# Optimization experiments

Measured on AMD Instinct MI355X. Metric: run time of the kernel, lower is better.

Reference implementation:

```python
import jax, jax.numpy as jnp
import numpy as np
from jax import lax

H = 1024      # hidden_size
E = 512       # embedding_size
K = 4         # max_num_children
NCLASS = 10000
EOS = NCLASS
N = 256       # number of tree nodes (complete K-ary tree, topo order)
L = 512       # number of annotation vectors


def setup_inputs() -> dict:
    key = jax.random.key(0)
    ks = jax.random.split(key, 16)
    s = 0.05
    rootH = jax.random.normal(ks[0], (1, H), jnp.float32)
    rootC = jax.random.normal(ks[1], (1, H), jnp.float32)
    annotations = jax.random.normal(ks[2], (L, H), jnp.float32)
    values = jax.random.randint(ks[3], (N,), 0, NCLASS, jnp.int32)
    idx = np.arange(N)
    parent = jnp.asarray(np.maximum(idx - 1, 0) // K, jnp.int32)
    slot = jnp.asarray(np.maximum(idx - 1, 0) % K, jnp.int32)
    # learned parameters
    emb = jax.random.normal(ks[4], (NCLASS + 1, E), jnp.float32) * s
    W_ih = jax.random.normal(ks[5], (K, 4 * H, E + H), jnp.float32) * s
    W_hh = jax.random.normal(ks[6], (K, 4 * H, H), jnp.float32) * s
    b_ih = jax.random.normal(ks[7], (K, 4 * H), jnp.float32) * s
    b_hh = jax.random.normal(ks[8], (K, 4 * H), jnp.float32) * s
    W_att = jax.random.normal(ks[9], (H, H), jnp.float32) * s
    b_att = jax.random.normal(ks[10], (H,), jnp.float32) * s
    W_pre = jax.random.normal(ks[11], (H, 2 * H), jnp.float32) * s
    b_pre = jax.random.normal(ks[12], (H,), jnp.float32) * s
    W_out = jax.random.normal(ks[13], (NCLASS + 1, H), jnp.float32) * s
    b_out = jax.random.normal(ks[14], (NCLASS + 1,), jnp.float32) * s
    return dict(rootH=rootH, rootC=rootC, annotations=annotations, values=values,
                parent=parent, slot=slot, emb=emb, W_ih=W_ih, W_hh=W_hh,
                b_ih=b_ih, b_hh=b_hh, W_att=W_att, b_att=b_att,
                W_pre=W_pre, b_pre=b_pre, W_out=W_out, b_out=b_out)


def reference(rootH, rootC, annotations, values, parent, slot, emb,
              W_ih, W_hh, b_ih, b_hh, W_att, b_att, W_pre, b_pre, W_out, b_out):
    # attention_hidden(annotations), computed once (align_type=1)
    ahv = annotations @ W_att.T + b_att            # [L, H]
    rootH0, rootC0 = rootH[0], rootC[0]            # [H]

    def step(carry, xs):
        Hbuf, Cbuf, etbuf, loss = carry
        i, v, p, k = xs
        # child LSTMCell update from parent state (slot k picks the cell)
        x = jnp.concatenate([emb[values[p]], etbuf[p]])            # [E+H]
        gates = W_ih[k] @ x + b_ih[k] + W_hh[k] @ Hbuf[p] + b_hh[k]  # [4H]
        ig, fg, gg, og = jnp.split(gates, 4)
        c_child = jax.nn.sigmoid(fg) * Cbuf[p] + jax.nn.sigmoid(ig) * jnp.tanh(gg)
        h_child = jax.nn.sigmoid(og) * jnp.tanh(c_child)
        is_root = i == 0
        h = jnp.where(is_root, rootH0, h_child)
        c = jnp.where(is_root, rootC0, c_child)
        # attention over annotations (softmax over L)
        att_logits = ahv @ h                                        # [L]
        probs = jax.nn.softmax(att_logits)
        ctx = probs @ annotations                                   # [H]
        et = jnp.tanh(W_pre @ jnp.concatenate([h, ctx]) + b_pre)    # [H]
        # output: softmax then CrossEntropyLoss (faithful double softmax)
        out_logits = W_out @ et + b_out                             # [NCLASS+1]
        p_out = jax.nn.softmax(out_logits)
        ls = jax.nn.log_softmax(p_out)
        nl = -ls[v]
        nl = jnp.where(v == EOS, nl / 5.0, nl)
        Hbuf = Hbuf.at[i].set(h)
        Cbuf = Cbuf.at[i].set(c)
        etbuf = etbuf.at[i].set(et)
        return (Hbuf, Cbuf, etbuf, loss + nl), None

    z = jnp.zeros((N, H), jnp.float32)
    init = (z, z, z, jnp.float32(0.0))
    xs = (jnp.arange(N, dtype=jnp.int32), values, parent, slot)
    (Hb, Cb, eb, loss), _ = lax.scan(step, init, xs)
    return loss
```

## Files before the change

### kernel.cpp

```cpp
#include <hip/hip_runtime.h>
#include <hip/hip_bf16.h>
#include <math.h>

#define HD 1024
#define NCLS 10001

typedef short s16x8 __attribute__((ext_vector_type(8)));
typedef unsigned short u16x8 __attribute__((ext_vector_type(8)));
typedef unsigned short u16x4 __attribute__((ext_vector_type(4)));
typedef float f32x4 __attribute__((ext_vector_type(4)));
#define MFMA16(a_, b_, c_) __builtin_amdgcn_mfma_f32_16x16x32_bf16((a_), (b_), (c_), 0, 0, 0)

__device__ __forceinline__ float sigf(float x){ return 1.f/(1.f+__expf(-x)); }
__device__ __forceinline__ float tanhfast(float x){
  x = fminf(fmaxf(x,-10.f),10.f);
  float e2 = __expf(2.f*x);
  return (e2-1.f)/(e2+1.f);
}
__device__ __forceinline__ unsigned short f2bf(float f){
  unsigned int u = __float_as_uint(f);
  u += 0x7FFF + ((u >> 16) & 1);
  return (unsigned short)(u >> 16);
}
__device__ __forceinline__ float bf2f(unsigned short u){
  return __uint_as_float(((unsigned)u) << 16);
}
__device__ __forceinline__ u16x8 pack8(float4 a, float4 b){
  u16x8 r;
  r[0]=f2bf(a.x); r[1]=f2bf(a.y); r[2]=f2bf(a.z); r[3]=f2bf(a.w);
  r[4]=f2bf(b.x); r[5]=f2bf(b.y); r[6]=f2bf(b.z); r[7]=f2bf(b.w);
  return r;
}

__global__ __launch_bounds__(256) void k_cvt32(const float* __restrict__ A, unsigned short* __restrict__ B, int n){
  int i = (blockIdx.x*256 + threadIdx.x)*32;
  if (i >= n) return;
  float4 a0 = *(const float4*)(A+i+ 0), b0 = *(const float4*)(A+i+ 4);
  float4 a1 = *(const float4*)(A+i+ 8), b1 = *(const float4*)(A+i+12);
  float4 a2 = *(const float4*)(A+i+16), b2 = *(const float4*)(A+i+20);
  float4 a3 = *(const float4*)(A+i+24), b3 = *(const float4*)(A+i+28);
  *(u16x8*)(B+i+ 0) = pack8(a0,b0);
  *(u16x8*)(B+i+ 8) = pack8(a1,b1);
  *(u16x8*)(B+i+16) = pack8(a2,b2);
  *(u16x8*)(B+i+24) = pack8(a3,b3);
}

__global__ __launch_bounds__(256) void k_cvtpre8(const float* __restrict__ Wpre,
                                                 unsigned short* __restrict__ Bpre, unsigned short* __restrict__ Wc){
  unsigned idx8 = (blockIdx.x*256 + threadIdx.x)*8;
  unsigned row = idx8 >> 11, c = idx8 & 2047;
  float4 a = *(const float4*)(Wpre + idx8);
  float4 b = *(const float4*)(Wpre + idx8 + 4);
  unsigned short* d = (c < 1024) ? (Bpre + (size_t)row*1536 + c) : (Wc + (size_t)row*1024 + (c-1024));
  *(u16x8*)d = pack8(a,b);
}

__global__ __launch_bounds__(256) void k_root(const float* __restrict__ rH, const float* __restrict__ rC,
                                              float* __restrict__ Hb, float* __restrict__ Cb,
                                              unsigned short* __restrict__ XH){
  int t = blockIdx.x*256 + threadIdx.x;
  if (t < HD){ Hb[t]=rH[t]; Cb[t]=rC[t]; XH[t]=f2bf(rH[t]); }
}

__global__ __launch_bounds__(256) void k_xasm(const float* __restrict__ emb, const int* __restrict__ values,
                                              const unsigned short* __restrict__ Etb, const unsigned short* __restrict__ XH,
                                              unsigned short* __restrict__ X, int s, int e){
  int i = s + blockIdx.x;
  if (i >= e) return;
  int slot = (i - s) & 3, j = (i - s) >> 2;
  int p = (i - 1) >> 2;
  unsigned short* xr = X + ((size_t)slot*48 + j) * 2560;
  int tid = threadIdx.x;
  if (tid < 64) {
    int c = tid*8;
    const float* er = emb + (size_t)values[p] * 512;
    float4 a = *(const float4*)(er+c);
    float4 b = *(const float4*)(er+c+4);
    *(u16x8*)(xr+c) = pack8(a,b);
  } else if (tid < 192) {
    int c = (tid-64)*8;
    const unsigned short* et = Etb + (size_t)p * 1024;
    *(u16x8*)(xr+512+c) = *(const u16x8*)(et+c);
  } else {
    int c = (tid-192)*16;
    const unsigned short* hp = XH + (size_t)p * 1536;
    *(u16x8*)(xr+1536+c)   = *(const u16x8*)(hp+c);
    *(u16x8*)(xr+1536+c+8) = *(const u16x8*)(hp+c+8);
  }
}

template<int MT>
__global__ __launch_bounds__(256) void k_gemm_fb(
    const unsigned short* __restrict__ A, int astride,
    const unsigned short* __restrict__ B, int K,
    const float* __restrict__ bias,
    float* __restrict__ Cf, unsigned short* __restrict__ Cb16,
    int ostride, int coff, int N, int M)
{
  const int mb0 = blockIdx.y * (MT*16);
  const int wv = threadIdx.x >> 6, lane = threadIdx.x & 63;
  const int col = (blockIdx.x*4 + wv)*16 + (lane & 15);
  const int colc = min(col, N-1);
  const int khalf = (lane >> 4) * 8;

  f32x4 acc[MT];
  #pragma unroll
  for (int m = 0; m < MT; ++m) acc[m] = (f32x4){0.f,0.f,0.f,0.f};
  int arow[MT];
  #pragma unroll
  for (int m = 0; m < MT; ++m) arow[m] = min(mb0 + m*16 + (lane & 15), M-1);

  #pragma unroll 4
  for (int kk = 0; kk < K; kk += 32) {
    int kb = kk + khalf;
    s16x8 bfv = *(const s16x8*)(B + (size_t)colc*K + kb);
    #pragma unroll
    for (int m = 0; m < MT; ++m) {
      s16x8 af = *(const s16x8*)(A + (size_t)arow[m]*astride + kb);
      acc[m] = MFMA16(af, bfv, acc[m]);
    }
  }

  const int r0 = (lane >> 4) * 4;
  #pragma unroll
  for (int m = 0; m < MT; ++m) {
    #pragma unroll
    for (int q = 0; q < 4; ++q) {
      int row = mb0 + m*16 + r0 + q;
      if (row < M && col < N) {
        float v = acc[m][q] + (bias ? bias[col] : 0.f);
        size_t off = (size_t)row*ostride + col + coff;
        if (Cb16) Cb16[off] = f2bf(v); else Cf[off] = v;
      }
    }
  }
}

__global__ __launch_bounds__(256) void k_wout(
    const unsigned short* __restrict__ A,
    const unsigned short* __restrict__ B,
    const float* __restrict__ bias,
    unsigned short* __restrict__ Lgb)
{
  __shared__ unsigned short bs[16*1032];
  const int c0 = blockIdx.x*16;
  const int tid = threadIdx.x;
  const unsigned short* src = B + (size_t)c0*1024;
  #pragma unroll
  for (int it = 0; it < 8; ++it) {
    int e = it*2048 + tid*8;
    int row = e >> 10, ck = e & 1023;
    *(u16x8*)(bs + row*1032 + ck) = *(const u16x8*)(src + e);
  }
  __syncthreads();

  const int wv = tid >> 6, lane = tid & 63;
  const int col16 = lane & 15;
  const int khalf = (lane >> 4) * 8;
  const int mb0 = wv * 64;
  const int col = c0 + col16;

  f32x4 acc[4];
  #pragma unroll
  for (int m=0;m<4;++m) acc[m] = (f32x4){0.f,0.f,0.f,0.f};
  int arow[4];
  #pragma unroll
  for (int m=0;m<4;++m) arow[m] = mb0 + m*16 + col16;

  #pragma unroll 8
  for (int kk = 0; kk < 1024; kk += 32) {
    int kb = kk + khalf;
    s16x8 bfv = *(const s16x8*)(bs + col16*1032 + kb);
    #pragma unroll
    for (int m=0;m<4;++m) {
      s16x8 af = *(const s16x8*)(A + (size_t)arow[m]*1024 + kb);
      acc[m] = MFMA16(af, bfv, acc[m]);
    }
  }

  if (col < NCLS) {
    const int r0 = (lane >> 4) * 4;
    float bv = bias[col];
    #pragma unroll
    for (int m=0;m<4;++m) {
      #pragma unroll
      for (int q=0;q<4;++q) {
        int row = mb0 + m*16 + r0 + q;
        Lgb[(size_t)row*NCLS + col] = f2bf(acc[m][q] + bv);
      }
    }
  }
}

template<int MT, int KITER>
__global__ __launch_bounds__(256) void k_gemm_skzb2(
    const unsigned short* __restrict__ A, int astride,
    const unsigned short* __restrict__ B1, int K1,
    const unsigned short* __restrict__ B2, int K2,
    float* __restrict__ P, int N, int Mbase, int Mpad,
    int aZ, int b1Z, int b2Z, int KS)
{
  const int z = blockIdx.z;
  const int M = (Mbase - z + 3) >> 2;
  const unsigned short* Az = A + (size_t)z*aZ;
  const unsigned short* B1z = B1 + (size_t)z*b1Z;
  const unsigned short* B2z = B2 + (size_t)z*b2Z;
  const int ks = blockIdx.y;
  const int k0 = ks * (KITER*32);
  const int wv = threadIdx.x >> 6, lane = threadIdx.x & 63;
  const int col = (blockIdx.x*4 + wv)*16 + (lane & 15);
  const int colc = min(col, N-1);
  const int khalf = (lane >> 4) * 8;

  f32x4 acc[MT];
  #pragma unroll
  for (int m = 0; m < MT; ++m) acc[m] = (f32x4){0.f,0.f,0.f,0.f};
  int arow[MT];
  #pragma unroll
  for (int m = 0; m < MT; ++m) arow[m] = min(m*16 + (lane & 15), M-1);

  #pragma unroll 8
  for (int kk = 0; kk < KITER*32; kk += 32) {
    int kb = k0 + kk + khalf;
    const unsigned short* bp = (kb < K1) ? (B1z + (size_t)colc*K1 + kb)
                                         : (B2z + (size_t)colc*K2 + (kb - K1));
    s16x8 bfv = *(const s16x8*)bp;
    #pragma unroll
    for (int m = 0; m < MT; ++m) {
      s16x8 af = *(const s16x8*)(Az + (size_t)arow[m]*astride + kb);
      acc[m] = MFMA16(af, bfv, acc[m]);
    }
  }

  const int r0 = (lane >> 4) * 4;
  #pragma unroll
  for (int m = 0; m < MT; ++m) {
    #pragma unroll
    for (int q = 0; q < 4; ++q) {
      int row = m*16 + r0 + q;
      if (row < M && col < N)
        P[(((size_t)z*KS + ks)*Mpad + row)*N + col] = acc[m][q];
    }
  }
}

template<int MT>
__global__ __launch_bounds__(256) void k_gemm_skb(
    const unsigned short* __restrict__ A, int astride,
    const unsigned short* __restrict__ B, int K,
    float* __restrict__ P, int N, int M)
{
  const int ks = blockIdx.y;
  const int k0 = ks * 128;
  const int wv = threadIdx.x >> 6, lane = threadIdx.x & 63;
  const int col = (blockIdx.x*4 + wv)*16 + (lane & 15);
  const int colc = min(col, N-1);
  const int khalf = (lane >> 4) * 8;

  f32x4 acc[MT];
  #pragma unroll
  for (int m = 0; m < MT; ++m) acc[m] = (f32x4){0.f,0.f,0.f,0.f};
  int arow[MT];
  #pragma unroll
  for (int m = 0; m < MT; ++m) arow[m] = min(m*16 + (lane & 15), M-1);

  #pragma unroll
  for (int kk = 0; kk < 128; kk += 32) {
    int kb = k0 + kk + khalf;
    s16x8 bfv = *(const s16x8*)(B + (size_t)colc*K + kb);
    #pragma unroll
    for (int m = 0; m < MT; ++m) {
      s16x8 af = *(const s16x8*)(A + (size_t)arow[m]*astride + kb);
      acc[m] = MFMA16(af, bfv, acc[m]);
    }
  }

  const int r0 = (lane >> 4) * 4;
  #pragma unroll
  for (int m = 0; m < MT; ++m) {
    #pragma unroll
    for (int q = 0; q < 4; ++q) {
      int row = m*16 + r0 + q;
      if (row < M && col < N)
        P[((size_t)ks*M + row)*N + col] = acc[m][q];
    }
  }
}

__global__ __launch_bounds__(256) void k_red4(const float* __restrict__ P, int KS, int M, int N,
                                              const float* __restrict__ bias, int tanh_flag,
                                              unsigned short* __restrict__ Cb16, int ostride)
{
  int idx4 = (blockIdx.x*256 + threadIdx.x)*4;
  if (idx4 >= M*N) return;
  int row = idx4 / N, col = idx4 - row*N;
  float4 s = *(const float4*)(bias + col);
  for (int ks = 0; ks < KS; ++ks) {
    float4 p = *(const float4*)(P + ((size_t)ks*M + row)*N + col);
    s.x += p.x; s.y += p.y; s.z += p.z; s.w += p.w;
  }
  if (tanh_flag){ s.x=tanhfast(s.x); s.y=tanhfast(s.y); s.z=tanhfast(s.z); s.w=tanhfast(s.w); }
  u16x4 r; r[0]=f2bf(s.x); r[1]=f2bf(s.y); r[2]=f2bf(s.z); r[3]=f2bf(s.w);
  *(u16x4*)(Cb16 + (size_t)row*ostride + col) = r;
}

__global__ __launch_bounds__(256) void k_soft(const float* __restrict__ P, int KS, int M,
                                              unsigned short* __restrict__ dst)
{
  __shared__ float sm[512];
  __shared__ float red[8];
  const int m = blockIdx.x;
  const int tid = threadIdx.x, wv = tid>>6, ln = tid&63;
  for (int l = tid; l < 512; l += 256) {
    float s = 0.f;
    for (int ks = 0; ks < KS; ++ks) s += P[((size_t)ks*M + m)*512 + l];
    sm[l] = s;
  }
  __syncthreads();
  float mx = -1e30f;
  for (int l=tid; l<512; l+=256) mx = fmaxf(mx, sm[l]);
  #pragma unroll
  for (int o=32;o;o>>=1) mx = fmaxf(mx, __shfl_xor(mx,o,64));
  if (ln==0) red[wv]=mx;
  __syncthreads();
  mx = fmaxf(fmaxf(red[0],red[1]),fmaxf(red[2],red[3]));
  float se = 0.f;
  for (int l=tid; l<512; l+=256){ float ev=__expf(sm[l]-mx); sm[l]=ev; se+=ev; }
  __syncthreads();
  #pragma unroll
  for (int o=32;o;o>>=1) se += __shfl_xor(se,o,64);
  if (ln==0) red[wv]=se;
  __syncthreads();
  float invS = 1.f/(red[0]+red[1]+red[2]+red[3]);
  for (int l=tid; l<512; l+=256) dst[(size_t)m*1536 + l] = f2bf(sm[l]*invS);
}

__global__ __launch_bounds__(256) void k_epi(const float* __restrict__ P,
                                             const float* __restrict__ b_ih, const float* __restrict__ b_hh,
                                             float* __restrict__ Hb, float* __restrict__ Cb,
                                             unsigned short* __restrict__ XH, int s, int e){
  int i = s + blockIdx.x;
  if (i >= e) return;
  int slot = (i - s) & 3, j = (i - s) >> 2;
  int p = (i - 1) >> 2;
  const float* bi = b_ih + (size_t)slot*4096;
  const float* bh = b_hh + (size_t)slot*4096;
  const int u = threadIdx.x*4;

  float4 ig, fg, gg, og;
  {
    float4 a, b;
    a = *(const float4*)(bi+u);      b = *(const float4*)(bh+u);      ig = make_float4(a.x+b.x,a.y+b.y,a.z+b.z,a.w+b.w);
    a = *(const float4*)(bi+1024+u); b = *(const float4*)(bh+1024+u); fg = make_float4(a.x+b.x,a.y+b.y,a.z+b.z,a.w+b.w);
    a = *(const float4*)(bi+2048+u); b = *(const float4*)(bh+2048+u); gg = make_float4(a.x+b.x,a.y+b.y,a.z+b.z,a.w+b.w);
    a = *(const float4*)(bi+3072+u); b = *(const float4*)(bh+3072+u); og = make_float4(a.x+b.x,a.y+b.y,a.z+b.z,a.w+b.w);
  }
  #pragma unroll
  for (int ks = 0; ks < 5; ++ks) {
    const float* g = P + (((size_t)slot*5 + ks)*48 + j)*4096;
    float4 a;
    a = *(const float4*)(g+u);      ig.x+=a.x; ig.y+=a.y; ig.z+=a.z; ig.w+=a.w;
    a = *(const float4*)(g+1024+u); fg.x+=a.x; fg.y+=a.y; fg.z+=a.z; fg.w+=a.w;
    a = *(const float4*)(g+2048+u); gg.x+=a.x; gg.y+=a.y; gg.z+=a.z; gg.w+=a.w;
    a = *(const float4*)(g+3072+u); og.x+=a.x; og.y+=a.y; og.z+=a.z; og.w+=a.w;
  }
  float4 cp = *(const float4*)(Cb + (size_t)p*1024 + u);
  float4 cc, hh;
  cc.x = sigf(fg.x)*cp.x + sigf(ig.x)*tanhfast(gg.x); hh.x = sigf(og.x)*tanhfast(cc.x);
  cc.y = sigf(fg.y)*cp.y + sigf(ig.y)*tanhfast(gg.y); hh.y = sigf(og.y)*tanhfast(cc.y);
  cc.z = sigf(fg.z)*cp.z + sigf(ig.z)*tanhfast(gg.z); hh.z = sigf(og.z)*tanhfast(cc.z);
  cc.w = sigf(fg.w)*cp.w + sigf(ig.w)*tanhfast(gg.w); hh.w = sigf(og.w)*tanhfast(cc.w);
  *(float4*)(Hb + (size_t)i*1024 + u) = hh;
  *(float4*)(Cb + (size_t)i*1024 + u) = cc;
  u16x4 r; r[0]=f2bf(hh.x); r[1]=f2bf(hh.y); r[2]=f2bf(hh.z); r[3]=f2bf(hh.w);
  *(u16x4*)(XH + (size_t)i*1536 + u) = r;
}

__global__ __launch_bounds__(256) void k_loss(const unsigned short* __restrict__ Lgb,
                                              const int* __restrict__ values,
                                              float* __restrict__ Nl)
{
  __shared__ float red[8];
  const int node = blockIdx.x;
  const int tid = threadIdx.x, wv = tid>>6, ln = tid&63;
  const unsigned short* lg = Lgb + (size_t)node*NCLS;

  float m = -1e30f;
  for (int i=tid;i<NCLS;i+=256) m = fmaxf(m, bf2f(lg[i]));
  #pragma unroll
  for (int o=32;o;o>>=1) m = fmaxf(m, __shfl_xor(m,o,64));
  if (ln==0) red[wv]=m;
  __syncthreads();
  m = fmaxf(fmaxf(red[0],red[1]),fmaxf(red[2],red[3]));
  __syncthreads();

  float s = 0.f;
  for (int i=tid;i<NCLS;i+=256) s += __expf(bf2f(lg[i])-m);
  #pragma unroll
  for (int o=32;o;o>>=1) s += __shfl_xor(s,o,64);
  if (ln==0) red[wv]=s;
  __syncthreads();
  s = red[0]+red[1]+red[2]+red[3];
  __syncthreads();
  float invs = 1.f/s;

  float q = 0.f;
  for (int i=tid;i<NCLS;i+=256) q += __expf(__expf(bf2f(lg[i])-m)*invs);
  #pragma unroll
  for (int o=32;o;o>>=1) q += __shfl_xor(q,o,64);
  if (ln==0) red[wv]=q;
  __syncthreads();
  if (tid==0) {
    float qq = red[0]+red[1]+red[2]+red[3];
    int v = values[node];
    float pv = __expf(bf2f(lg[v])-m)*invs;
    float nl = __logf(qq) - pv;
    if (v == NCLS-1) nl *= 0.2f;
    Nl[node] = nl;
  }
}

__global__ __launch_bounds__(256) void k_final(const float* __restrict__ Nl, float* __restrict__ out){
  __shared__ float red[8];
  int tid = threadIdx.x, wv = tid>>6, ln = tid&63;
  float s = Nl[tid];
  #pragma unroll
  for (int o=32;o;o>>=1) s += __shfl_xor(s,o,64);
  if (ln==0) red[wv]=s;
  __syncthreads();
  if (tid==0) out[0] = red[0]+red[1]+red[2]+red[3];
}

static inline void gemm_skb(hipStream_t st, int MT, const unsigned short* A, int astride,
                            const unsigned short* B, int K, float* P, int N, int M)
{
  dim3 grid(N/64, K/128);
  #define SKCASE(MTv) k_gemm_skb<MTv><<<grid, 256, 0, st>>>(A,astride,B,K,P,N,M)
  switch(MT){
    case 1:  SKCASE(1);  break;
    case 4:  SKCASE(4);  break;
    case 11: SKCASE(11); break;
    default: SKCASE(16); break;
  }
  #undef SKCASE
}

extern "C" void kernel_launch(void* const* d_in, const int* in_sizes, int n_in,
                              void* d_out, int out_size, void* d_ws, size_t ws_size,
                              hipStream_t stream)
{
  const float* rootH = (const float*)d_in[0];
  const float* rootC = (const float*)d_in[1];
  const float* ann   = (const float*)d_in[2];
  const int*   values= (const int*)d_in[3];
  const float* emb   = (const float*)d_in[6];
  const float* W_ih  = (const float*)d_in[7];
  const float* W_hh  = (const float*)d_in[8];
  const float* b_ih  = (const float*)d_in[9];
  const float* b_hh  = (const float*)d_in[10];
  const float* W_att = (const float*)d_in[11];
  const float* b_att = (const float*)d_in[12];
  const float* W_pre = (const float*)d_in[13];
  const float* b_pre = (const float*)d_in[14];
  const float* W_out = (const float*)d_in[15];
  const float* b_out = (const float*)d_in[16];

  float* ws = (float*)d_ws;
  float* Hb  = ws; ws += 256*1024;
  float* Cb  = ws; ws += 256*1024;
  float* Nl  = ws; ws += 256;
  float* PB  = ws; ws += 4*5*48*4096;
  unsigned short* Wbih  = (unsigned short*)ws;
  unsigned short* Wbhh  = Wbih  + (size_t)4*4096*1536;
  unsigned short* Woutb = Wbhh  + (size_t)4*4096*1024;
  unsigned short* Wattb = Woutb + (size_t)NCLS*1024;
  unsigned short* Bpre  = Wattb + 1024*1024;
  unsigned short* Wpcb  = Bpre  + 1024*1536;
  unsigned short* AHVb  = Wpcb  + 1024*1024;
  unsigned short* Annb  = AHVb  + 512*1024;
  unsigned short* XH    = Annb  + 512*1024;
  unsigned short* Etb   = XH    + 256*1536;
  unsigned short* Xb    = Etb   + 256*1024;
  unsigned short* Lgb   = Xb    + 4*48*2560;

  k_cvt32 <<<3072, 256, 0, stream>>>(W_ih,  Wbih,  4*4096*1536);
  k_cvt32 <<<2048, 256, 0, stream>>>(W_hh,  Wbhh,  4*4096*1024);
  k_cvt32 <<<1251, 256, 0, stream>>>(W_out, Woutb, NCLS*1024);
  k_cvt32 <<<64,   256, 0, stream>>>(ann,   Annb,  512*1024);
  k_cvt32 <<<128,  256, 0, stream>>>(W_att, Wattb, 1024*1024);
  k_cvtpre8<<<1024, 256, 0, stream>>>(W_pre, Bpre, Wpcb);
  k_gemm_fb<4><<<dim3(16,8),  256, 0, stream>>>(Annb, 1024, Wattb, 1024, b_att, nullptr, AHVb, 1024, 0, 1024, 512);
  k_gemm_fb<4><<<dim3(8,16),  256, 0, stream>>>(Wpcb, 1024, Annb, 1024, nullptr, nullptr, Bpre, 1536, 1024, 512, 1024);
  k_root<<<4, 256, 0, stream>>>(rootH, rootC, Hb, Cb, XH);

  const int LS[6] = {0,1,5,21,85,256};
  for (int lev=0; lev<5; ++lev){
    int s=LS[lev], e=LS[lev+1], n=e-s;
    if (lev>0){
      k_xasm<<<n,256,0,stream>>>(emb, values, Etb, XH, Xb, s, e);
      if (lev==4)
        k_gemm_skzb2<3,16><<<dim3(64,5,4),256,0,stream>>>(Xb, 2560, Wbih, 1536, Wbhh, 1024, PB,
            4096, n, 48, 48*2560, 4096*1536, 4096*1024, 5);
      else
        k_gemm_skzb2<1,16><<<dim3(64,5,4),256,0,stream>>>(Xb, 2560, Wbih, 1536, Wbhh, 1024, PB,
            4096, n, 48, 48*2560, 4096*1536, 4096*1024, 5);
      k_epi<<<n,256,0,stream>>>(PB, b_ih, b_hh, Hb, Cb, XH, s, e);
    }
    int mtn = (n+15)/16;
    gemm_skb(stream, mtn, XH + (size_t)s*1536, 1536, AHVb, 1024, PB, 512, n);
    k_soft<<<n,256,0,stream>>>(PB, 8, n, XH + (size_t)s*1536 + 1024);
    gemm_skb(stream, mtn, XH + (size_t)s*1536, 1536, Bpre, 1536, PB, 1024, n);
    k_red4<<<(n*1024/4+255)/256, 256, 0, stream>>>(PB, 12, n, 1024, b_pre, 1, Etb + (size_t)s*1024, 1024);
  }

  k_wout<<<626, 256, 0, stream>>>(Etb, Woutb, b_out, Lgb);
  k_loss <<<256,256,0,stream>>>(Lgb, values, Nl);
  k_final<<<1,  256,0,stream>>>(Nl, (float*)d_out);
}
```

Measured before the change: 447.4 us.

## Fuse conversions, scatter child inputs from epilogues, and fuse attention logits with softmax

Six weight-conversion launches are merged into one kernel. Embedding rows are gathered for all levels once up front. The per-level x-assembly kernel is dropped because the LSTM epilogue and the W_pre reduction now write h and et straight into the next level's per-level input buffer. The attention split-K GEMM plus softmax pair becomes one k_att kernel that computes the 512 logits with scalar FMAs from bf16 AHV and applies the softmax. Together these cut serial kernel launches per tree level and remove intermediate round trips. In exchange the attention dot products move off MFMA onto a per-node block that rereads the 1 MB AHV matrix.

```diff
diff --git a/kernel.cpp b/kernel.cpp
--- a/kernel.cpp
+++ b/kernel.cpp
@@ -32,61 +32,67 @@
   return r;
 }
 
-__global__ __launch_bounds__(256) void k_cvt32(const float* __restrict__ A, unsigned short* __restrict__ B, int n){
-  int i = (blockIdx.x*256 + threadIdx.x)*32;
-  if (i >= n) return;
-  float4 a0 = *(const float4*)(A+i+ 0), b0 = *(const float4*)(A+i+ 4);
-  float4 a1 = *(const float4*)(A+i+ 8), b1 = *(const float4*)(A+i+12);
-  float4 a2 = *(const float4*)(A+i+16), b2 = *(const float4*)(A+i+20);
-  float4 a3 = *(const float4*)(A+i+24), b3 = *(const float4*)(A+i+28);
-  *(u16x8*)(B+i+ 0) = pack8(a0,b0);
-  *(u16x8*)(B+i+ 8) = pack8(a1,b1);
-  *(u16x8*)(B+i+16) = pack8(a2,b2);
-  *(u16x8*)(B+i+24) = pack8(a3,b3);
-}
-
-__global__ __launch_bounds__(256) void k_cvtpre8(const float* __restrict__ Wpre,
-                                                 unsigned short* __restrict__ Bpre, unsigned short* __restrict__ Wc){
-  unsigned idx8 = (blockIdx.x*256 + threadIdx.x)*8;
-  unsigned row = idx8 >> 11, c = idx8 & 2047;
-  float4 a = *(const float4*)(Wpre + idx8);
-  float4 b = *(const float4*)(Wpre + idx8 + 4);
-  unsigned short* d = (c < 1024) ? (Bpre + (size_t)row*1536 + c) : (Wc + (size_t)row*1024 + (c-1024));
-  *(u16x8*)d = pack8(a,b);
+#define CN0 25165824
+#define CN1 16777216
+#define CN2 10241024
+#define CN3 524288
+#define CN4 1048576
+#define CN5 2097152
+__global__ __launch_bounds__(256) void k_cvtall(
+    const float* __restrict__ Wih, const float* __restrict__ Whh, const float* __restrict__ Wout,
+    const float* __restrict__ ann, const float* __restrict__ Watt, const float* __restrict__ Wpre,
+    unsigned short* __restrict__ Wbih, unsigned short* __restrict__ Wbhh, unsigned short* __restrict__ Woutb,
+    unsigned short* __restrict__ Annb, unsigned short* __restrict__ Wattb,
+    unsigned short* __restrict__ Bpre, unsigned short* __restrict__ Wpcb)
+{
+  unsigned idx = (blockIdx.x*256 + threadIdx.x)*32u;
+  const float* src; unsigned short* dst;
+  if (idx < CN0) { src = Wih + idx; dst = Wbih + idx; }
+  else if ((idx -= CN0) < CN1) { src = Whh + idx; dst = Wbhh + idx; }
+  else if ((idx -= CN1) < CN2) { src = Wout + idx; dst = Woutb + idx; }
+  else if ((idx -= CN2) < CN3) { src = ann + idx; dst = Annb + idx; }
+  else if ((idx -= CN3) < CN4) { src = Watt + idx; dst = Wattb + idx; }
+  else if ((idx -= CN4) < CN5) {
+    src = Wpre + idx;
+    unsigned row = idx >> 11, c = idx & 2047;
+    dst = (c < 1024) ? (Bpre + (size_t)row*1536 + c) : (Wpcb + (size_t)row*1024 + (c-1024));
+  } else return;
+  #pragma unroll
+  for (int t = 0; t < 4; ++t) {
+    float4 a = *(const float4*)(src + t*8);
+    float4 b = *(const float4*)(src + t*8 + 4);
+    *(u16x8*)(dst + t*8) = pack8(a,b);
+  }
+}
+
+__global__ __launch_bounds__(64) void k_emb(const float* __restrict__ emb, const int* __restrict__ values,
+                                            unsigned short* __restrict__ Xb){
+  int i = blockIdx.x + 1;
+  int lev, s;
+  if (i < 5)       { lev=1; s=1; }
+  else if (i < 21) { lev=2; s=5; }
+  else if (i < 85) { lev=3; s=21; }
+  else             { lev=4; s=85; }
+  int p = (i-1)>>2, o = i - s;
+  unsigned short* xr = Xb + ((size_t)(lev-1)*4*48 + (size_t)(o&3)*48 + (o>>2)) * 2560;
+  const float* er = emb + (size_t)values[p]*512;
+  int c = threadIdx.x*8;
+  float4 a = *(const float4*)(er+c), b = *(const float4*)(er+c+4);
+  *(u16x8*)(xr+c) = pack8(a,b);
 }
 
 __global__ __launch_bounds__(256) void k_root(const float* __restrict__ rH, const float* __restrict__ rC,
-                                              float* __restrict__ Hb, float* __restrict__ Cb,
-                                              unsigned short* __restrict__ XH){
-  int t = blockIdx.x*256 + threadIdx.x;
-  if (t < HD){ Hb[t]=rH[t]; Cb[t]=rC[t]; XH[t]=f2bf(rH[t]); }
-}
-
-__global__ __launch_bounds__(256) void k_xasm(const float* __restrict__ emb, const int* __restrict__ values,
-                                              const unsigned short* __restrict__ Etb, const unsigned short* __restrict__ XH,
-                                              unsigned short* __restrict__ X, int s, int e){
-  int i = s + blockIdx.x;
-  if (i >= e) return;
-  int slot = (i - s) & 3, j = (i - s) >> 2;
-  int p = (i - 1) >> 2;
-  unsigned short* xr = X + ((size_t)slot*48 + j) * 2560;
-  int tid = threadIdx.x;
-  if (tid < 64) {
-    int c = tid*8;
-    const float* er = emb + (size_t)values[p] * 512;
-    float4 a = *(const float4*)(er+c);
-    float4 b = *(const float4*)(er+c+4);
-    *(u16x8*)(xr+c) = pack8(a,b);
-  } else if (tid < 192) {
-    int c = (tid-64)*8;
-    const unsigned short* et = Etb + (size_t)p * 1024;
-    *(u16x8*)(xr+512+c) = *(const u16x8*)(et+c);
-  } else {
-    int c = (tid-192)*16;
-    const unsigned short* hp = XH + (size_t)p * 1536;
-    *(u16x8*)(xr+1536+c)   = *(const u16x8*)(hp+c);
-    *(u16x8*)(xr+1536+c+8) = *(const u16x8*)(hp+c+8);
-  }
+                                              float* __restrict__ Cb, unsigned short* __restrict__ XH,
+                                              unsigned short* __restrict__ Xb1){
+  int u = threadIdx.x*4;
+  float4 h = *(const float4*)(rH+u);
+  float4 c = *(const float4*)(rC+u);
+  *(float4*)(Cb+u) = c;
+  u16x4 r; r[0]=f2bf(h.x); r[1]=f2bf(h.y); r[2]=f2bf(h.z); r[3]=f2bf(h.w);
+  *(u16x4*)(XH+u) = r;
+  #pragma unroll
+  for (int k=0;k<4;++k)
+    *(u16x4*)(Xb1 + (size_t)k*48*2560 + 1536 + u) = r;
 }
 
 template<int MT>
@@ -94,7 +100,7 @@
     const unsigned short* __restrict__ A, int astride,
     const unsigned short* __restrict__ B, int K,
     const float* __restrict__ bias,
-    float* __restrict__ Cf, unsigned short* __restrict__ Cb16,
+    unsigned short* __restrict__ Cb16,
     int ostride, int coff, int N, int M)
 {
   const int mb0 = blockIdx.y * (MT*16);
@@ -129,8 +135,7 @@
       int row = mb0 + m*16 + r0 + q;
       if (row < M && col < N) {
         float v = acc[m][q] + (bias ? bias[col] : 0.f);
-        size_t off = (size_t)row*ostride + col + coff;
-        if (Cb16) Cb16[off] = f2bf(v); else Cf[off] = v;
+        Cb16[(size_t)row*ostride + col + coff] = f2bf(v);
       }
     }
   }
@@ -287,60 +292,92 @@
   }
 }
 
-__global__ __launch_bounds__(256) void k_red4(const float* __restrict__ P, int KS, int M, int N,
-                                              const float* __restrict__ bias, int tanh_flag,
-                                              unsigned short* __restrict__ Cb16, int ostride)
-{
-  int idx4 = (blockIdx.x*256 + threadIdx.x)*4;
-  if (idx4 >= M*N) return;
-  int row = idx4 / N, col = idx4 - row*N;
-  float4 s = *(const float4*)(bias + col);
+__global__ __launch_bounds__(256) void k_red4(const float* __restrict__ P, int KS, int M,
+                                              const float* __restrict__ bias,
+                                              unsigned short* __restrict__ Etb, int s,
+                                              int snext, unsigned short* __restrict__ XbNext)
+{
+  const int row = blockIdx.x;
+  const int col = threadIdx.x*4;
+  float4 sum = *(const float4*)(bias + col);
   for (int ks = 0; ks < KS; ++ks) {
-    float4 p = *(const float4*)(P + ((size_t)ks*M + row)*N + col);
-    s.x += p.x; s.y += p.y; s.z += p.z; s.w += p.w;
-  }
-  if (tanh_flag){ s.x=tanhfast(s.x); s.y=tanhfast(s.y); s.z=tanhfast(s.z); s.w=tanhfast(s.w); }
-  u16x4 r; r[0]=f2bf(s.x); r[1]=f2bf(s.y); r[2]=f2bf(s.z); r[3]=f2bf(s.w);
-  *(u16x4*)(Cb16 + (size_t)row*ostride + col) = r;
-}
-
-__global__ __launch_bounds__(256) void k_soft(const float* __restrict__ P, int KS, int M,
-                                              unsigned short* __restrict__ dst)
-{
+    float4 p = *(const float4*)(P + ((size_t)ks*M + row)*1024 + col);
+    sum.x += p.x; sum.y += p.y; sum.z += p.z; sum.w += p.w;
+  }
+  u16x4 r;
+  r[0]=f2bf(tanhfast(sum.x)); r[1]=f2bf(tanhfast(sum.y));
+  r[2]=f2bf(tanhfast(sum.z)); r[3]=f2bf(tanhfast(sum.w));
+  *(u16x4*)(Etb + (size_t)(s+row)*1024 + col) = r;
+  if (XbNext) {
+    int cbase = 4*(s+row) + 1;
+    #pragma unroll
+    for (int k=0;k<4;++k) {
+      int cn = cbase + k;
+      if (cn < 256) {
+        int o = cn - snext;
+        *(u16x4*)(XbNext + ((size_t)(o&3)*48 + (o>>2))*2560 + 512 + col) = r;
+      }
+    }
+  }
+}
+
+__global__ __launch_bounds__(256) void k_att(const unsigned short* __restrict__ XH,
+                                             const unsigned short* __restrict__ AHVb, int s)
+{
+  __shared__ float hsh[1024];
   __shared__ float sm[512];
   __shared__ float red[8];
-  const int m = blockIdx.x;
+  const int node = s + blockIdx.x;
   const int tid = threadIdx.x, wv = tid>>6, ln = tid&63;
-  for (int l = tid; l < 512; l += 256) {
-    float s = 0.f;
-    for (int ks = 0; ks < KS; ++ks) s += P[((size_t)ks*M + m)*512 + l];
-    sm[l] = s;
-  }
-  __syncthreads();
-  float mx = -1e30f;
-  for (int l=tid; l<512; l+=256) mx = fmaxf(mx, sm[l]);
+  {
+    int c = tid*4;
+    u16x4 v = *(const u16x4*)(XH + (size_t)node*1536 + c);
+    hsh[c]=bf2f(v[0]); hsh[c+1]=bf2f(v[1]); hsh[c+2]=bf2f(v[2]); hsh[c+3]=bf2f(v[3]);
+  }
+  __syncthreads();
+
+  {
+    const unsigned short* b0 = AHVb + (size_t)tid*1024;
+    const unsigned short* b1 = AHVb + (size_t)(tid+256)*1024;
+    float a0 = 0.f, a1 = 0.f;
+    #pragma unroll 2
+    for (int k = 0; k < 1024; k += 8) {
+      u16x8 v0 = *(const u16x8*)(b0+k);
+      u16x8 v1 = *(const u16x8*)(b1+k);
+      #pragma unroll
+      for (int j=0;j<8;++j) {
+        float hv = hsh[k+j];
+        a0 = fmaf(bf2f(v0[j]), hv, a0);
+        a1 = fmaf(bf2f(v1[j]), hv, a1);
+      }
+    }
+    sm[tid] = a0; sm[tid+256] = a1;
+  }
+  __syncthreads();
+
+  float mx = fmaxf(sm[tid], sm[tid+256]);
   #pragma unroll
   for (int o=32;o;o>>=1) mx = fmaxf(mx, __shfl_xor(mx,o,64));
   if (ln==0) red[wv]=mx;
   __syncthreads();
   mx = fmaxf(fmaxf(red[0],red[1]),fmaxf(red[2],red[3]));
-  float se = 0.f;
-  for (int l=tid; l<512; l+=256){ float ev=__expf(sm[l]-mx); sm[l]=ev; se+=ev; }
-  __syncthreads();
+  float e0 = __expf(sm[tid]-mx), e1 = __expf(sm[tid+256]-mx);
+  float se = e0 + e1;
   #pragma unroll
   for (int o=32;o;o>>=1) se += __shfl_xor(se,o,64);
   if (ln==0) red[wv]=se;
   __syncthreads();
   float invS = 1.f/(red[0]+red[1]+red[2]+red[3]);
-  for (int l=tid; l<512; l+=256) dst[(size_t)m*1536 + l] = f2bf(sm[l]*invS);
+  unsigned short* dst = (unsigned short*)(XH + (size_t)node*1536 + 1024);
+  dst[tid]     = f2bf(e0*invS);
+  dst[tid+256] = f2bf(e1*invS);
 }
 
 __global__ __launch_bounds__(256) void k_epi(const float* __restrict__ P,
                                              const float* __restrict__ b_ih, const float* __restrict__ b_hh,
-                                             float* __restrict__ Hb, float* __restrict__ Cb,
-                                             unsigned short* __restrict__ XH, int s, int e){
+                                             float* __restrict__ Cb, unsigned short* __restrict__ XH,
+                                             int s, int snext, unsigned short* __restrict__ XbNext){
   int i = s + blockIdx.x;
-  if (i >= e) return;
   int slot = (i - s) & 3, j = (i - s) >> 2;
   int p = (i - 1) >> 2;
   const float* bi = b_ih + (size_t)slot*4096;
@@ -370,10 +407,20 @@
   cc.y = sigf(fg.y)*cp.y + sigf(ig.y)*tanhfast(gg.y); hh.y = sigf(og.y)*tanhfast(cc.y);
   cc.z = sigf(fg.z)*cp.z + sigf(ig.z)*tanhfast(gg.z); hh.z = sigf(og.z)*tanhfast(cc.z);
   cc.w = sigf(fg.w)*cp.w + sigf(ig.w)*tanhfast(gg.w); hh.w = sigf(og.w)*tanhfast(cc.w);
-  *(float4*)(Hb + (size_t)i*1024 + u) = hh;
   *(float4*)(Cb + (size_t)i*1024 + u) = cc;
   u16x4 r; r[0]=f2bf(hh.x); r[1]=f2bf(hh.y); r[2]=f2bf(hh.z); r[3]=f2bf(hh.w);
   *(u16x4*)(XH + (size_t)i*1536 + u) = r;
+  if (XbNext) {
+    int cbase = 4*i + 1;
+    #pragma unroll
+    for (int k=0;k<4;++k) {
+      int cn = cbase + k;
+      if (cn < 256) {
+        int o = cn - snext;
+        *(u16x4*)(XbNext + ((size_t)(o&3)*48 + (o>>2))*2560 + 1536 + u) = r;
+      }
+    }
+  }
 }
 
 __global__ __launch_bounds__(256) void k_loss(const unsigned short* __restrict__ Lgb,
@@ -466,7 +513,6 @@
   const float* b_out = (const float*)d_in[16];
 
   float* ws = (float*)d_ws;
-  float* Hb  = ws; ws += 256*1024;
   float* Cb  = ws; ws += 256*1024;
   float* Nl  = ws; ws += 256;
   float* PB  = ws; ws += 4*5*48*4096;
@@ -481,36 +527,34 @@
   unsigned short* XH    = Annb  + 512*1024;
   unsigned short* Etb   = XH    + 256*1536;
   unsigned short* Xb    = Etb   + 256*1024;
-  unsigned short* Lgb   = Xb    + 4*48*2560;
-
-  k_cvt32 <<<3072, 256, 0, stream>>>(W_ih,  Wbih,  4*4096*1536);
-  k_cvt32 <<<2048, 256, 0, stream>>>(W_hh,  Wbhh,  4*4096*1024);
-  k_cvt32 <<<1251, 256, 0, stream>>>(W_out, Woutb, NCLS*1024);
-  k_cvt32 <<<64,   256, 0, stream>>>(ann,   Annb,  512*1024);
-  k_cvt32 <<<128,  256, 0, stream>>>(W_att, Wattb, 1024*1024);
-  k_cvtpre8<<<1024, 256, 0, stream>>>(W_pre, Bpre, Wpcb);
-  k_gemm_fb<4><<<dim3(16,8),  256, 0, stream>>>(Annb, 1024, Wattb, 1024, b_att, nullptr, AHVb, 1024, 0, 1024, 512);
-  k_gemm_fb<4><<<dim3(8,16),  256, 0, stream>>>(Wpcb, 1024, Annb, 1024, nullptr, nullptr, Bpre, 1536, 1024, 512, 1024);
-  k_root<<<4, 256, 0, stream>>>(rootH, rootC, Hb, Cb, XH);
+  unsigned short* Lgb   = Xb    + (size_t)4*4*48*2560;
+
+  k_cvtall<<<6819, 256, 0, stream>>>(W_ih, W_hh, W_out, ann, W_att, W_pre,
+                                     Wbih, Wbhh, Woutb, Annb, Wattb, Bpre, Wpcb);
+  k_emb   <<<255,  64,  0, stream>>>(emb, values, Xb);
+  k_gemm_fb<4><<<dim3(16,8), 256, 0, stream>>>(Annb, 1024, Wattb, 1024, b_att, AHVb, 1024, 0, 1024, 512);
+  k_gemm_fb<4><<<dim3(8,16), 256, 0, stream>>>(Wpcb, 1024, Annb, 1024, nullptr, Bpre, 1536, 1024, 512, 1024);
+  k_root<<<1, 256, 0, stream>>>(rootH, rootC, Cb, XH, Xb);
 
   const int LS[6] = {0,1,5,21,85,256};
   for (int lev=0; lev<5; ++lev){
     int s=LS[lev], e=LS[lev+1], n=e-s;
+    unsigned short* XbL = Xb + (size_t)(lev-1)*4*48*2560;
+    unsigned short* XbN = (lev<4) ? (Xb + (size_t)lev*4*48*2560) : nullptr;
+    int snext = (lev<4) ? LS[lev+1] : 0;
     if (lev>0){
-      k_xasm<<<n,256,0,stream>>>(emb, values, Etb, XH, Xb, s, e);
       if (lev==4)
-        k_gemm_skzb2<3,16><<<dim3(64,5,4),256,0,stream>>>(Xb, 2560, Wbih, 1536, Wbhh, 1024, PB,
+        k_gemm_skzb2<3,16><<<dim3(64,5,4),256,0,stream>>>(XbL, 2560, Wbih, 1536, Wbhh, 1024, PB,
             4096, n, 48, 48*2560, 4096*1536, 4096*1024, 5);
       else
-        k_gemm_skzb2<1,16><<<dim3(64,5,4),256,0,stream>>>(Xb, 2560, Wbih, 1536, Wbhh, 1024, PB,
+        k_gemm_skzb2<1,16><<<dim3(64,5,4),256,0,stream>>>(XbL, 2560, Wbih, 1536, Wbhh, 1024, PB,
             4096, n, 48, 48*2560, 4096*1536, 4096*1024, 5);
-      k_epi<<<n,256,0,stream>>>(PB, b_ih, b_hh, Hb, Cb, XH, s, e);
-    }
+      k_epi<<<n,256,0,stream>>>(PB, b_ih, b_hh, Cb, XH, s, snext, XbN);
+    }
+    k_att<<<n,256,0,stream>>>(XH, AHVb, s);
     int mtn = (n+15)/16;
-    gemm_skb(stream, mtn, XH + (size_t)s*1536, 1536, AHVb, 1024, PB, 512, n);
-    k_soft<<<n,256,0,stream>>>(PB, 8, n, XH + (size_t)s*1536 + 1024);
     gemm_skb(stream, mtn, XH + (size_t)s*1536, 1536, Bpre, 1536, PB, 1024, n);
-    k_red4<<<(n*1024/4+255)/256, 256, 0, stream>>>(PB, 12, n, 1024, b_pre, 1, Etb + (size_t)s*1024, 1024);
+    k_red4<<<n,256,0,stream>>>(PB, 12, n, b_pre, Etb, s, snext, XbN);
   }
 
   k_wout<<<626, 256, 0, stream>>>(Etb, Woutb, b_out, Lgb);
```

New measurement: 562.9 us. 1.26x slower.
